# Performance work log

Measured on AMD Instinct MI355X. Metric: run time of the kernel, lower is better.

The kernel has to match this reference:

```python
import jax, jax.numpy as jnp
import numpy as np

B, N, D_IN, D_OUT = 16, 2048, 512, 512


def setup_inputs() -> dict:
    key = jax.random.key(0)
    ks = jax.random.split(key, 7)
    s = 1.0 / np.sqrt(D_IN)
    return {
        "x": jax.random.normal(ks[0], (B, N, D_IN), dtype=jnp.float32),
        "Wq": jax.random.uniform(ks[1], (D_IN, D_OUT), jnp.float32, -s, s),
        "bq": jax.random.uniform(ks[2], (D_OUT,), jnp.float32, -s, s),
        "Wk": jax.random.uniform(ks[3], (D_IN, D_OUT), jnp.float32, -s, s),
        "bk": jax.random.uniform(ks[4], (D_OUT,), jnp.float32, -s, s),
        "Wv": jax.random.uniform(ks[5], (D_IN, D_OUT), jnp.float32, -s, s),
        "bv": jax.random.uniform(ks[6], (D_OUT,), jnp.float32, -s, s),
    }


def reference(x, Wq, bq, Wk, bk, Wv, bv):
    # Q/K/V projections: [B,N,D]
    q = jnp.einsum("bnd,de->bne", x, Wq) + bq
    k = jnp.einsum("bnd,de->bne", x, Wk) + bk
    v = jnp.einsum("bnd,de->bne", x, Wv) + bv
    # Full NxN attention, no scaling (faithful to the original module)
    scores = jnp.einsum("bqe,bke->bqk", q, k)
    attn = jax.nn.softmax(scores, axis=-1)
    return jnp.einsum("bqk,bke->bqe", attn, v)
```

## Files before the change

### kernel.cpp

```cpp
#include <hip/hip_runtime.h>

typedef _Float16 half8  __attribute__((ext_vector_type(8)));
typedef _Float16 half4_t __attribute__((ext_vector_type(4)));
typedef float    f32x4  __attribute__((ext_vector_type(4)));

static constexpr int BATCH = 16;
static constexpr int NSEQ  = 2048;
static constexpr int DDIM  = 512;
static constexpr int MROWS = BATCH * NSEQ;

static constexpr size_t WT_OFF  = 0;
static constexpr size_t QKV_OFF = 2u * 1024 * 1024;
static constexpr size_t VT_OFF  = QKV_OFF + (size_t)3 * MROWS * DDIM * 2;

typedef const __attribute__((address_space(1))) void cg_void;
typedef __attribute__((address_space(3))) void lds_void;
__device__ __forceinline__ void gload_lds16(const void* g, void* l) {
    __builtin_amdgcn_global_load_lds((cg_void*)g, (lds_void*)l, 16, 0, 0);
}

__global__ void xconv(const float* __restrict__ x, _Float16* __restrict__ xh) {
    size_t base = ((size_t)blockIdx.x * 256 + threadIdx.x) * 8;
    float4 a = *(const float4*)(x + base);
    float4 b = *(const float4*)(x + base + 4);
    half8 h;
    h[0] = (_Float16)a.x; h[1] = (_Float16)a.y; h[2] = (_Float16)a.z; h[3] = (_Float16)a.w;
    h[4] = (_Float16)b.x; h[5] = (_Float16)b.y; h[6] = (_Float16)b.z; h[7] = (_Float16)b.w;
    *(half8*)(xh + base) = h;
}

__global__ void wt_prep(const float* __restrict__ Wq, const float* __restrict__ Wk,
                        const float* __restrict__ Wv, _Float16* __restrict__ wt) {
    int idx = blockIdx.x * 256 + threadIdx.x;
    int ng  = idx >> 9;
    int e   = idx & 511;
    const float* W = (ng < 512) ? Wq : (ng < 1024 ? Wk : Wv);
    wt[idx] = (_Float16)W[e * 512 + (ng & 511)];
}

__global__ __launch_bounds__(256, 2) void qkv_gemm(
        const _Float16* __restrict__ xh, const _Float16* __restrict__ wt,
        const float* __restrict__ bq, const float* __restrict__ bk,
        const float* __restrict__ bv, _Float16* __restrict__ qkv) {
    __shared__ alignas(16) char Asw[128 * 128];
    __shared__ alignas(16) char Bsw[128 * 128];
    const int tid  = threadIdx.x;
    const int lane = tid & 63;
    const int wid  = tid >> 6;
    const int lg = lane >> 4, lm = lane & 15;
    const int wr = wid >> 1, wc = wid & 1;

    const int id = blockIdx.x;
    const int wg = (id & 7) * 384 + (id >> 3);
    const int bm = wg & 255, bn = wg >> 8;
    const int m0 = bm * 128, n0 = bn * 128;
    const int proj = n0 >> 9;
    const float* bias = (proj == 0) ? bq : (proj == 1 ? bk : bv);

    f32x4 acc[4][4] = {};

    const int rloc = (lane >> 3);
    const int p    = lane & 7;

    for (int kk = 0; kk < 512; kk += 64) {
        __syncthreads();
        #pragma unroll
        for (int i = 0; i < 4; ++i) {
            int g = wid * 4 + i;
            int r = g * 8 + rloc;
            gload_lds16(xh + (size_t)(m0 + r) * 512 + kk + ((p ^ (r & 7)) * 8),
                        Asw + g * 1024);
            gload_lds16(wt + (size_t)(n0 + r) * 512 + kk + ((p ^ (r & 7)) * 8),
                        Bsw + g * 1024);
        }
        __syncthreads();
        #pragma unroll
        for (int es = 0; es < 2; ++es) {
            half8 a[4], b[4];
            #pragma unroll
            for (int i = 0; i < 4; ++i) {
                int row = wr * 64 + i * 16 + lm;
                a[i] = *(const half8*)(Asw + row * 128 + (((es * 4 + lg) ^ (row & 7)) * 16));
            }
            #pragma unroll
            for (int j = 0; j < 4; ++j) {
                int row = wc * 64 + j * 16 + lm;
                b[j] = *(const half8*)(Bsw + row * 128 + (((es * 4 + lg) ^ (row & 7)) * 16));
            }
            #pragma unroll
            for (int i = 0; i < 4; ++i)
                #pragma unroll
                for (int j = 0; j < 4; ++j)
                    acc[i][j] = __builtin_amdgcn_mfma_f32_16x16x32_f16(a[i], b[j], acc[i][j], 0, 0, 0);
        }
    }
    const size_t pb = (size_t)proj * MROWS * DDIM;
    #pragma unroll
    for (int i = 0; i < 4; ++i) {
        #pragma unroll
        for (int j = 0; j < 4; ++j) {
            int mg = m0 + wr * 64 + i * 16 + lg * 4;
            int c  = (n0 & 511) + wc * 64 + j * 16 + lm;
            float bb = bias[c];
            #pragma unroll
            for (int r = 0; r < 4; ++r)
                qkv[pb + (size_t)(mg + r) * DDIM + c] = (_Float16)(acc[i][j][r] + bb);
        }
    }
}

__global__ void v_transpose(const _Float16* __restrict__ v, _Float16* __restrict__ vt) {
    __shared__ alignas(16) _Float16 T[64][72];
    const int b = blockIdx.z;
    const int n0 = blockIdx.x * 64, e0 = blockIdx.y * 64;
    const int tid = threadIdx.x;
    #pragma unroll
    for (int i = 0; i < 2; ++i) {
        int c = tid + i * 256;
        int row = c >> 3, o = c & 7;
        int4 val = *(const int4*)(v + ((size_t)b * NSEQ + n0 + row) * 512 + e0 + o * 8);
        *(int4*)&T[row][o * 8] = val;
    }
    __syncthreads();
    #pragma unroll
    for (int i = 0; i < 2; ++i) {
        int c = tid + i * 256;
        int erow = c >> 3, o = c & 7;
        _Float16 tmp[8];
        #pragma unroll
        for (int j = 0; j < 8; ++j) tmp[j] = T[o * 8 + j][erow];
        *(int4*)(vt + (size_t)b * 512 * NSEQ + (size_t)(e0 + erow) * NSEQ + n0 + o * 8) =
            *(int4*)tmp;
    }
}

__global__ __launch_bounds__(512, 2) void attn(
        const _Float16* __restrict__ q, const _Float16* __restrict__ k,
        const _Float16* __restrict__ vt, float* __restrict__ out) {
    __shared__ alignas(16) char smem[2 * 32768 + 2 * 32768 + 8 * 16 * 40 * 2];
    char* KsB = smem;
    char* VsB = smem + 65536;
    _Float16 (*Pl)[16][40] = (_Float16 (*)[16][40])(smem + 131072);

    const int tid = threadIdx.x, lane = tid & 63, wid = tid >> 6;
    const int lg = lane >> 4, lm = lane & 15;
    const int id = blockIdx.x;
    const int b  = id & 15;
    const int n0 = (id >> 4) * 128;

    const _Float16* qrow = q + ((size_t)(b * NSEQ + n0 + wid * 16 + lm)) * 512;
    half8 qf[16];
    #pragma unroll
    for (int es = 0; es < 16; ++es)
        qf[es] = *(const half8*)(qrow + es * 32 + lg * 8);

    f32x4 o[32] = {};
    float m_r[4], l_r[4];
    #pragma unroll
    for (int r = 0; r < 4; ++r) { m_r[r] = -__builtin_inff(); l_r[r] = 0.f; }

    const _Float16* kb  = k  + (size_t)b * NSEQ * 512;
    const _Float16* vtb = vt + (size_t)b * 512 * NSEQ;

    int koff[4], voff[4];
    #pragma unroll
    for (int i = 0; i < 4; ++i) {
        int R = wid * 4 + i;
        koff[i] = R * 512 + ((lane ^ (R & 7)) * 8);
        voff[i] = (R * 16 + (lane >> 2)) * NSEQ + (((lane & 3) ^ ((lane >> 3) & 3)) * 8);
    }

    #pragma unroll
    for (int i = 0; i < 4; ++i) {
        gload_lds16(kb + koff[i], KsB + (wid * 4 + i) * 1024);
        gload_lds16(vtb + voff[i], VsB + (wid * 4 + i) * 1024);
    }

    int buf = 0;
    for (int t = 0; t < 64; ++t) {
        __syncthreads();
        if (t < 63) {
            const _Float16* ks = kb + (size_t)(t + 1) * (32 * 512);
            const _Float16* vs = vtb + (size_t)(t + 1) * 32;
            const int nb = buf ^ 1;
            #pragma unroll
            for (int i = 0; i < 4; ++i) {
                gload_lds16(ks + koff[i], KsB + nb * 32768 + (wid * 4 + i) * 1024);
                gload_lds16(vs + voff[i], VsB + nb * 32768 + (wid * 4 + i) * 1024);
            }
        }
        const char* Ksb = KsB + buf * 32768;
        const char* Vsb = VsB + buf * 32768;

        f32x4 s0 = {}, s1 = {};
        #pragma unroll
        for (int es = 0; es < 16; ++es) {
            const int off = es * 64 + lg * 16;
            half8 k0 = *(const half8*)(Ksb + lm * 1024 + (off ^ ((lm & 7) << 4)));
            half8 k1 = *(const half8*)(Ksb + (lm + 16) * 1024 + (off ^ ((lm & 7) << 4)));
            s0 = __builtin_amdgcn_mfma_f32_16x16x32_f16(qf[es], k0, s0, 0, 0, 0);
            s1 = __builtin_amdgcn_mfma_f32_16x16x32_f16(qf[es], k1, s1, 0, 0, 0);
        }

        float sc[4], p0[4], p1[4];
        #pragma unroll
        for (int r = 0; r < 4; ++r) {
            float tm = fmaxf(s0[r], s1[r]);
            #pragma unroll
            for (int d = 1; d < 16; d <<= 1) tm = fmaxf(tm, __shfl_xor(tm, d));
            float mn = fmaxf(m_r[r], tm);
            sc[r] = __expf(m_r[r] - mn);
            p0[r] = __expf(s0[r] - mn);
            p1[r] = __expf(s1[r] - mn);
            float rsum = p0[r] + p1[r];
            #pragma unroll
            for (int d = 1; d < 16; d <<= 1) rsum += __shfl_xor(rsum, d);
            l_r[r] = l_r[r] * sc[r] + rsum;
            m_r[r] = mn;
        }
        #pragma unroll
        for (int eg = 0; eg < 32; ++eg)
            #pragma unroll
            for (int r = 0; r < 4; ++r) o[eg][r] *= sc[r];

        #pragma unroll
        for (int r = 0; r < 4; ++r) {
            Pl[wid][lg * 4 + r][lm]      = (_Float16)p0[r];
            Pl[wid][lg * 4 + r][lm + 16] = (_Float16)p1[r];
        }
        half8 pf = *(const half8*)&Pl[wid][lm][lg * 8];

        #pragma unroll
        for (int eg = 0; eg < 32; ++eg) {
            int e = eg * 16 + lm;
            half8 vf = *(const half8*)(Vsb + e * 64 + ((lg ^ ((lm >> 1) & 3)) << 4));
            o[eg] = __builtin_amdgcn_mfma_f32_16x16x32_f16(pf, vf, o[eg], 0, 0, 0);
        }
        buf ^= 1;
    }

    float inv[4];
    #pragma unroll
    for (int r = 0; r < 4; ++r) inv[r] = 1.f / l_r[r];
    float* ob = out + ((size_t)(b * NSEQ + n0 + wid * 16 + lg * 4)) * 512;
    #pragma unroll
    for (int eg = 0; eg < 32; ++eg)
        #pragma unroll
        for (int r = 0; r < 4; ++r)
            ob[(size_t)r * 512 + eg * 16 + lm] = o[eg][r] * inv[r];
}

extern "C" void kernel_launch(void* const* d_in, const int* in_sizes, int n_in,
                              void* d_out, int out_size, void* d_ws, size_t ws_size,
                              hipStream_t stream) {
    const float* x  = (const float*)d_in[0];
    const float* Wq = (const float*)d_in[1];
    const float* bq = (const float*)d_in[2];
    const float* Wk = (const float*)d_in[3];
    const float* bk = (const float*)d_in[4];
    const float* Wv = (const float*)d_in[5];
    const float* bv = (const float*)d_in[6];
    float* out = (float*)d_out;
    char* ws = (char*)d_ws;

    _Float16* wt   = (_Float16*)(ws + WT_OFF);
    _Float16* qkv  = (_Float16*)(ws + QKV_OFF);
    _Float16* qbuf = qkv;
    _Float16* kbuf = qkv + (size_t)1 * MROWS * DDIM;
    _Float16* vbuf = qkv + (size_t)2 * MROWS * DDIM;
    _Float16* vt   = (_Float16*)(ws + VT_OFF);
    _Float16* xh   = (_Float16*)(ws + VT_OFF);

    xconv<<<8192, 256, 0, stream>>>(x, xh);
    wt_prep<<<(1536 * 512) / 256, 256, 0, stream>>>(Wq, Wk, Wv, wt);
    qkv_gemm<<<3072, 256, 0, stream>>>(xh, wt, bq, bk, bv, qkv);
    v_transpose<<<dim3(NSEQ / 64, DDIM / 64, BATCH), 256, 0, stream>>>(vbuf, vt);
    attn<<<256, 512, 0, stream>>>(qbuf, kbuf, vt, out);
}
```

Before: 469.1 us.

## Split attention PV across warps by output column with shared P tile

Restructures the attention kernel to 64-query blocks of 4 warps. Each warp still computes QK scores for its own 16 rows, but the P tile and rescale factors are shared through LDS so each warp does the PV product for all 64 rows over a 128-column slice of V. This cuts per-warp V LDS reads and the accumulator register count, and doubles the grid to 512 blocks. K/V double buffering is replaced by single buffers with K prefetch issued after a mid-iteration barrier, which adds a second sync per step and less overlap of the V load.

```diff
diff --git a/kernel.cpp b/kernel.cpp
--- a/kernel.cpp
+++ b/kernel.cpp
@@ -134,19 +134,20 @@
     }
 }
 
-__global__ __launch_bounds__(512, 2) void attn(
+__global__ __launch_bounds__(256, 2) void attn(
         const _Float16* __restrict__ q, const _Float16* __restrict__ k,
         const _Float16* __restrict__ vt, float* __restrict__ out) {
-    __shared__ alignas(16) char smem[2 * 32768 + 2 * 32768 + 8 * 16 * 40 * 2];
-    char* KsB = smem;
-    char* VsB = smem + 65536;
-    _Float16 (*Pl)[16][40] = (_Float16 (*)[16][40])(smem + 131072);
+    __shared__ alignas(16) char Ks[32 * 1024];
+    __shared__ alignas(16) char Vs[32 * 1024];
+    __shared__ alignas(16) char Ps[64 * 64];
+    __shared__ alignas(16) float scA[64];
 
     const int tid = threadIdx.x, lane = tid & 63, wid = tid >> 6;
     const int lg = lane >> 4, lm = lane & 15;
+
     const int id = blockIdx.x;
-    const int b  = id & 15;
-    const int n0 = (id >> 4) * 128;
+    const int b  = (id & 7) * 2 + (id >> 8);
+    const int n0 = ((id >> 3) & 31) * 64;
 
     const _Float16* qrow = q + ((size_t)(b * NSEQ + n0 + wid * 16 + lm)) * 512;
     half8 qf[16];
@@ -154,7 +155,7 @@
     for (int es = 0; es < 16; ++es)
         qf[es] = *(const half8*)(qrow + es * 32 + lg * 8);
 
-    f32x4 o[32] = {};
+    f32x4 o[4][8] = {};
     float m_r[4], l_r[4];
     #pragma unroll
     for (int r = 0; r < 4; ++r) { m_r[r] = -__builtin_inff(); l_r[r] = 0.f; }
@@ -162,42 +163,33 @@
     const _Float16* kb  = k  + (size_t)b * NSEQ * 512;
     const _Float16* vtb = vt + (size_t)b * 512 * NSEQ;
 
-    int koff[4], voff[4];
-    #pragma unroll
-    for (int i = 0; i < 4; ++i) {
-        int R = wid * 4 + i;
+    int koff[8], voff[8];
+    #pragma unroll
+    for (int i = 0; i < 8; ++i) {
+        int R = wid * 8 + i;
         koff[i] = R * 512 + ((lane ^ (R & 7)) * 8);
         voff[i] = (R * 16 + (lane >> 2)) * NSEQ + (((lane & 3) ^ ((lane >> 3) & 3)) * 8);
     }
 
     #pragma unroll
-    for (int i = 0; i < 4; ++i) {
-        gload_lds16(kb + koff[i], KsB + (wid * 4 + i) * 1024);
-        gload_lds16(vtb + voff[i], VsB + (wid * 4 + i) * 1024);
-    }
-
-    int buf = 0;
+    for (int i = 0; i < 8; ++i)
+        gload_lds16(kb + koff[i], Ks + (wid * 8 + i) * 1024);
+
     for (int t = 0; t < 64; ++t) {
         __syncthreads();
-        if (t < 63) {
-            const _Float16* ks = kb + (size_t)(t + 1) * (32 * 512);
-            const _Float16* vs = vtb + (size_t)(t + 1) * 32;
-            const int nb = buf ^ 1;
-            #pragma unroll
-            for (int i = 0; i < 4; ++i) {
-                gload_lds16(ks + koff[i], KsB + nb * 32768 + (wid * 4 + i) * 1024);
-                gload_lds16(vs + voff[i], VsB + nb * 32768 + (wid * 4 + i) * 1024);
-            }
-        }
-        const char* Ksb = KsB + buf * 32768;
-        const char* Vsb = VsB + buf * 32768;
+        {
+            const _Float16* vs = vtb + t * 32;
+            #pragma unroll
+            for (int i = 0; i < 8; ++i)
+                gload_lds16(vs + voff[i], Vs + (wid * 8 + i) * 1024);
+        }
 
         f32x4 s0 = {}, s1 = {};
         #pragma unroll
         for (int es = 0; es < 16; ++es) {
             const int off = es * 64 + lg * 16;
-            half8 k0 = *(const half8*)(Ksb + lm * 1024 + (off ^ ((lm & 7) << 4)));
-            half8 k1 = *(const half8*)(Ksb + (lm + 16) * 1024 + (off ^ ((lm & 7) << 4)));
+            half8 k0 = *(const half8*)(Ks + lm * 1024 + (off ^ ((lm & 7) << 4)));
+            half8 k1 = *(const half8*)(Ks + (lm + 16) * 1024 + (off ^ ((lm & 7) << 4)));
             s0 = __builtin_amdgcn_mfma_f32_16x16x32_f16(qf[es], k0, s0, 0, 0, 0);
             s1 = __builtin_amdgcn_mfma_f32_16x16x32_f16(qf[es], k1, s1, 0, 0, 0);
         }
@@ -218,36 +210,73 @@
             l_r[r] = l_r[r] * sc[r] + rsum;
             m_r[r] = mn;
         }
-        #pragma unroll
-        for (int eg = 0; eg < 32; ++eg)
-            #pragma unroll
-            for (int r = 0; r < 4; ++r) o[eg][r] *= sc[r];
 
         #pragma unroll
         for (int r = 0; r < 4; ++r) {
-            Pl[wid][lg * 4 + r][lm]      = (_Float16)p0[r];
-            Pl[wid][lg * 4 + r][lm + 16] = (_Float16)p1[r];
-        }
-        half8 pf = *(const half8*)&Pl[wid][lm][lg * 8];
-
-        #pragma unroll
-        for (int eg = 0; eg < 32; ++eg) {
-            int e = eg * 16 + lm;
-            half8 vf = *(const half8*)(Vsb + e * 64 + ((lg ^ ((lm >> 1) & 3)) << 4));
-            o[eg] = __builtin_amdgcn_mfma_f32_16x16x32_f16(pf, vf, o[eg], 0, 0, 0);
-        }
-        buf ^= 1;
-    }
-
-    float inv[4];
-    #pragma unroll
-    for (int r = 0; r < 4; ++r) inv[r] = 1.f / l_r[r];
-    float* ob = out + ((size_t)(b * NSEQ + n0 + wid * 16 + lg * 4)) * 512;
-    #pragma unroll
-    for (int eg = 0; eg < 32; ++eg)
-        #pragma unroll
-        for (int r = 0; r < 4; ++r)
-            ob[(size_t)r * 512 + eg * 16 + lm] = o[eg][r] * inv[r];
+            int row = wid * 16 + lg * 4 + r;
+            *(_Float16*)(Ps + row * 64 + (((lm >> 3) ^ lg) << 4) + (lm & 7) * 2) = (_Float16)p0[r];
+            *(_Float16*)(Ps + row * 64 + (((2 + (lm >> 3)) ^ lg) << 4) + (lm & 7) * 2) = (_Float16)p1[r];
+        }
+        if (lm == 0) {
+            f32x4 scv; scv[0] = sc[0]; scv[1] = sc[1]; scv[2] = sc[2]; scv[3] = sc[3];
+            *(f32x4*)&scA[wid * 16 + lg * 4] = scv;
+        }
+
+        __syncthreads();
+
+        if (t < 63) {
+            const _Float16* ks2 = kb + (size_t)(t + 1) * (32 * 512);
+            #pragma unroll
+            for (int i = 0; i < 8; ++i)
+                gload_lds16(ks2 + koff[i], Ks + (wid * 8 + i) * 1024);
+        }
+
+        #pragma unroll
+        for (int m = 0; m < 4; ++m) {
+            f32x4 scv = *(const f32x4*)&scA[m * 16 + lg * 4];
+            #pragma unroll
+            for (int eg = 0; eg < 8; ++eg)
+                #pragma unroll
+                for (int r = 0; r < 4; ++r) o[m][eg][r] *= scv[r];
+        }
+
+        half8 vf[8];
+        #pragma unroll
+        for (int eg = 0; eg < 8; ++eg) {
+            int e = wid * 128 + eg * 16 + lm;
+            vf[eg] = *(const half8*)(Vs + e * 64 + ((lg ^ ((lm >> 1) & 3)) << 4));
+        }
+        #pragma unroll
+        for (int m = 0; m < 4; ++m) {
+            int row = m * 16 + lm;
+            half8 pf = *(const half8*)(Ps + row * 64 + ((lg ^ ((lm >> 2) & 3)) << 4));
+            #pragma unroll
+            for (int eg = 0; eg < 8; ++eg)
+                o[m][eg] = __builtin_amdgcn_mfma_f32_16x16x32_f16(pf, vf[eg], o[m][eg], 0, 0, 0);
+        }
+    }
+
+    __syncthreads();
+    if (lm == 0) {
+        f32x4 lv; lv[0] = l_r[0]; lv[1] = l_r[1]; lv[2] = l_r[2]; lv[3] = l_r[3];
+        *(f32x4*)&scA[wid * 16 + lg * 4] = lv;
+    }
+    __syncthreads();
+    #pragma unroll
+    for (int m = 0; m < 4; ++m) {
+        f32x4 lv = *(const f32x4*)&scA[m * 16 + lg * 4];
+        float inv[4];
+        #pragma unroll
+        for (int r = 0; r < 4; ++r) inv[r] = __builtin_amdgcn_rcpf(lv[r]);
+        #pragma unroll
+        for (int eg = 0; eg < 8; ++eg) {
+            #pragma unroll
+            for (int r = 0; r < 4; ++r) {
+                out[((size_t)(b * NSEQ + n0 + m * 16 + lg * 4 + r)) * 512
+                    + wid * 128 + eg * 16 + lm] = o[m][eg][r] * inv[r];
+            }
+        }
+    }
 }
 
 extern "C" void kernel_launch(void* const* d_in, const int* in_sizes, int n_in,
@@ -275,5 +304,5 @@
     wt_prep<<<(1536 * 512) / 256, 256, 0, stream>>>(Wq, Wk, Wv, wt);
     qkv_gemm<<<3072, 256, 0, stream>>>(xh, wt, bq, bk, bv, qkv);
     v_transpose<<<dim3(NSEQ / 64, DDIM / 64, BATCH), 256, 0, stream>>>(vbuf, vt);
-    attn<<<256, 512, 0, stream>>>(qbuf, kbuf, vt, out);
-}
+    attn<<<512, 256, 0, stream>>>(qbuf, kbuf, vt, out);
+}
```

Result: slower. 566.9 us (+20.8%).

## Deepen K/V prefetch pipeline, add lazy softmax rescale, priority hints, and block swizzle

Applied to the files above, without the earlier changes.

The attention loop now issues two tiles of K/V loads up front and waits with explicit vmcnt counts, so the next tile's loads stay in flight across the barrier instead of a full syncthreads drain. The online softmax skips rescaling the accumulator unless the running max grows by more than a threshold, and the 32 accumulator multiplies run only if some lane in the wavefront needs them. MFMA sections are wrapped in s_setprio, and the block index mapping is permuted so concurrently running blocks group batches differently for cache locality. The lazy-max trick relies on fp16 P values not overflowing when exponent differences stay up to 8. The manual vmcnt and barrier sequencing is fragile if the compiler reorders loads.

```diff
diff --git a/kernel.cpp b/kernel.cpp
--- a/kernel.cpp
+++ b/kernel.cpp
@@ -137,16 +137,16 @@
 __global__ __launch_bounds__(512, 2) void attn(
         const _Float16* __restrict__ q, const _Float16* __restrict__ k,
         const _Float16* __restrict__ vt, float* __restrict__ out) {
-    __shared__ alignas(16) char smem[2 * 32768 + 2 * 32768 + 8 * 16 * 40 * 2];
-    char* KsB = smem;
-    char* VsB = smem + 65536;
-    _Float16 (*Pl)[16][40] = (_Float16 (*)[16][40])(smem + 131072);
+    __shared__ alignas(16) char KsB[2 * 32768];
+    __shared__ alignas(16) char VsB[2 * 32768];
+    __shared__ alignas(16) _Float16 Pl[8][16][40];
 
     const int tid = threadIdx.x, lane = tid & 63, wid = tid >> 6;
     const int lg = lane >> 4, lm = lane & 15;
+
     const int id = blockIdx.x;
-    const int b  = id & 15;
-    const int n0 = (id >> 4) * 128;
+    const int b  = (id & 7) | ((id >> 7) << 3);
+    const int n0 = ((id >> 3) & 15) * 128;
 
     const _Float16* qrow = q + ((size_t)(b * NSEQ + n0 + wid * 16 + lm)) * 512;
     half8 qf[16];
@@ -170,29 +170,29 @@
         voff[i] = (R * 16 + (lane >> 2)) * NSEQ + (((lane & 3) ^ ((lane >> 3) & 3)) * 8);
     }
 
-    #pragma unroll
-    for (int i = 0; i < 4; ++i) {
-        gload_lds16(kb + koff[i], KsB + (wid * 4 + i) * 1024);
-        gload_lds16(vtb + voff[i], VsB + (wid * 4 + i) * 1024);
-    }
-
-    int buf = 0;
+    auto STAGE = [&](int tt, int bb) {
+        const _Float16* ks = kb + (size_t)tt * (32 * 512);
+        const _Float16* vs = vtb + (size_t)tt * 32;
+        #pragma unroll
+        for (int i = 0; i < 4; ++i) {
+            gload_lds16(ks + koff[i], KsB + bb * 32768 + (wid * 4 + i) * 1024);
+            gload_lds16(vs + voff[i], VsB + bb * 32768 + (wid * 4 + i) * 1024);
+        }
+    };
+
+    STAGE(0, 0);
+    STAGE(1, 1);
+
     for (int t = 0; t < 64; ++t) {
-        __syncthreads();
-        if (t < 63) {
-            const _Float16* ks = kb + (size_t)(t + 1) * (32 * 512);
-            const _Float16* vs = vtb + (size_t)(t + 1) * 32;
-            const int nb = buf ^ 1;
-            #pragma unroll
-            for (int i = 0; i < 4; ++i) {
-                gload_lds16(ks + koff[i], KsB + nb * 32768 + (wid * 4 + i) * 1024);
-                gload_lds16(vs + voff[i], VsB + nb * 32768 + (wid * 4 + i) * 1024);
-            }
-        }
-        const char* Ksb = KsB + buf * 32768;
-        const char* Vsb = VsB + buf * 32768;
+        if (t < 62) asm volatile("s_waitcnt vmcnt(8)" ::: "memory");
+        else        asm volatile("s_waitcnt vmcnt(0)" ::: "memory");
+        __builtin_amdgcn_s_barrier();
+
+        const char* Ksb = KsB + (t & 1) * 32768;
+        const char* Vsb = VsB + (t & 1) * 32768;
 
         f32x4 s0 = {}, s1 = {};
+        __builtin_amdgcn_s_setprio(1);
         #pragma unroll
         for (int es = 0; es < 16; ++es) {
             const int off = es * 64 + lg * 16;
@@ -201,27 +201,29 @@
             s0 = __builtin_amdgcn_mfma_f32_16x16x32_f16(qf[es], k0, s0, 0, 0, 0);
             s1 = __builtin_amdgcn_mfma_f32_16x16x32_f16(qf[es], k1, s1, 0, 0, 0);
         }
+        __builtin_amdgcn_s_setprio(0);
 
         float sc[4], p0[4], p1[4];
+        bool resc = false;
         #pragma unroll
         for (int r = 0; r < 4; ++r) {
             float tm = fmaxf(s0[r], s1[r]);
             #pragma unroll
             for (int d = 1; d < 16; d <<= 1) tm = fmaxf(tm, __shfl_xor(tm, d));
             float mn = fmaxf(m_r[r], tm);
-            sc[r] = __expf(m_r[r] - mn);
-            p0[r] = __expf(s0[r] - mn);
-            p1[r] = __expf(s1[r] - mn);
+            float use_m;
+            if (mn - m_r[r] <= 8.f) {
+                use_m = m_r[r]; sc[r] = 1.f;
+            } else {
+                use_m = mn; sc[r] = __expf(m_r[r] - mn); m_r[r] = mn; resc = true;
+            }
+            p0[r] = __expf(s0[r] - use_m);
+            p1[r] = __expf(s1[r] - use_m);
             float rsum = p0[r] + p1[r];
             #pragma unroll
             for (int d = 1; d < 16; d <<= 1) rsum += __shfl_xor(rsum, d);
             l_r[r] = l_r[r] * sc[r] + rsum;
-            m_r[r] = mn;
-        }
-        #pragma unroll
-        for (int eg = 0; eg < 32; ++eg)
-            #pragma unroll
-            for (int r = 0; r < 4; ++r) o[eg][r] *= sc[r];
+        }
 
         #pragma unroll
         for (int r = 0; r < 4; ++r) {
@@ -230,13 +232,25 @@
         }
         half8 pf = *(const half8*)&Pl[wid][lm][lg * 8];
 
+        if (__any((int)resc)) {
+            #pragma unroll
+            for (int eg = 0; eg < 32; ++eg)
+                #pragma unroll
+                for (int r = 0; r < 4; ++r) o[eg][r] *= sc[r];
+        }
+
+        __builtin_amdgcn_s_setprio(1);
         #pragma unroll
         for (int eg = 0; eg < 32; ++eg) {
             int e = eg * 16 + lm;
             half8 vf = *(const half8*)(Vsb + e * 64 + ((lg ^ ((lm >> 1) & 3)) << 4));
             o[eg] = __builtin_amdgcn_mfma_f32_16x16x32_f16(pf, vf, o[eg], 0, 0, 0);
         }
-        buf ^= 1;
+        __builtin_amdgcn_s_setprio(0);
+
+        __builtin_amdgcn_s_barrier();
+        asm volatile("" ::: "memory");
+        if (t + 2 < 64) STAGE(t + 2, t & 1);
     }
 
     float inv[4];
```

Measured after the change: 528.9 us. +12.7%, slower.
